# Optimization experiments

Hardware: AMD Instinct MI355X
Metric: run time of the kernel (lower is better)

Reference implementation:

```python
import jax, jax.numpy as jnp
import numpy as np

EPSILON = 0.1
ITERATIONS = 5
GAMMA = 0.1
TAU = 0.005
NEG = -1000000.0
DELTA = 1e-9


def setup_inputs() -> dict:
    key = jax.random.key(0)
    kv, kt, klv, klt = jax.random.split(key, 4)
    B, n_v, n_t, dim = 64, 512, 512, 768
    v = jax.random.normal(kv, (B, n_v, dim), dtype=jnp.float32)
    t = jax.random.normal(kt, (B, n_t, dim), dtype=jnp.float32)
    # realistic length-based masks (prefix-valid tokens), at least half valid
    len_v = jax.random.randint(klv, (B,), n_v // 2, n_v + 1)
    len_t = jax.random.randint(klt, (B,), n_t // 2, n_t + 1)
    v_mask = jnp.arange(n_v)[None, :] < len_v[:, None]
    t_mask = jnp.arange(n_t)[None, :] < len_t[:, None]
    return {"v": v, "t": t, "v_mask": v_mask, "t_mask": t_mask}


def _l2norm(x):
    return x / jnp.sqrt(jnp.sum(x * x, axis=-1, keepdims=True)).clip(1e-12)


def reference(v, t, v_mask, t_mask):
    B, n_v, dim = v.shape
    n_t = t.shape[1]
    # cosine similarity scores: [B, n_v, n_t]
    A = jnp.einsum("bvd,btd->bvt", _l2norm(v), _l2norm(t)).astype(jnp.float32)
    A_raw = A
    A = jnp.where(v_mask[:, :, None], A, NEG)
    A = jnp.where(t_mask[:, None, :], A, NEG)

    gamma = jnp.float32(GAMMA)
    def augment(M):
        M = jnp.concatenate([M, jnp.full((B, n_v, 1), gamma, M.dtype)], axis=2)
        M = jnp.concatenate([M, jnp.full((B, 1, n_t + 1), gamma, M.dtype)], axis=1)
        return M
    A_aug = augment(A)          # [B, n_v+1, n_t+1]
    A_aug_raw = augment(A_raw)

    mu_real = v_mask.astype(jnp.float32) / (v_mask.sum(axis=1, keepdims=True) + 1e-9)
    nu_real = t_mask.astype(jnp.float32) / (t_mask.sum(axis=1, keepdims=True) + 1e-9)
    ones = jnp.ones((B, 1), jnp.float32)
    mu = jnp.concatenate([mu_real, ones], axis=1)  # [B, n_v+1]
    nu = jnp.concatenate([nu_real, ones], axis=1)  # [B, n_t+1]

    K = A_aug / EPSILON
    log_mu = jnp.log(mu + 1e-9)
    log_nu = jnp.log(nu + 1e-9)

    def step(carry, _):
        u, vv = carry
        u = log_mu - jax.nn.logsumexp(K + vv[:, None, :], axis=2)
        vv = log_nu - jax.nn.logsumexp(K + u[:, :, None], axis=1)
        return (u, vv), None

    u0 = jnp.zeros_like(mu)
    v0 = jnp.zeros_like(nu)
    (u, vv), _ = jax.lax.scan(step, (u0, v0), None, length=ITERATIONS)

    log_T = u[:, :, None] + vv[:, None, :] + K
    T_star = jnp.exp(log_T)
    loss = jnp.sum(T_star * (1.0 - A_aug_raw), axis=(1, 2))

    T_real = T_star[:, :n_v, :n_t]
    T_hat = jax.nn.relu(T_real - TAU)
    w_v_num = T_hat.sum(axis=2) + DELTA
    w_v = w_v_num / w_v_num.sum(axis=1, keepdims=True)
    w_t_num = T_hat.sum(axis=1) + DELTA
    w_t = w_t_num / w_t_num.sum(axis=1, keepdims=True)
    return (loss.mean(), w_v, w_t)
```

## Files before the change

### kernel.cpp

```cpp
#include <hip/hip_runtime.h>
#include <hip/hip_fp16.h>

#define TAU_OT   0.005f
#define DELTA_OT 1e-9f
#define LOG2E    1.4426950408889634f
#define C_EPS    0.06931471805599453f
#define LM9_2    -29.897352853986263f
#define NEGI     -1.0e30f
#define SCALE_B  14.426950408889634f

constexpr int BB  = 64;
constexpr int DIM = 768;
constexpr int KP_H = 520;
constexpr long KB_H = (long)512 * KP_H;

constexpr size_t OFF_LENV = 0;
constexpr size_t OFF_LENT = 64;
constexpr size_t OFF_SCAL = 128;
constexpr size_t OFF_LOSSA= 384;
constexpr size_t OFF_SRU  = 448;
constexpr size_t OFF_SRV  = 512;
constexpr size_t OFF_U    = 576;
constexpr size_t OFF_VV   = OFF_U   + 32768;
constexpr size_t OFF_WVA  = OFF_VV  + 32768;
constexpr size_t OFF_WTA  = OFF_WVA + 32768;
constexpr size_t OFF_KH   = OFF_WTA + 32768;

typedef __attribute__((ext_vector_type(8))) short short8;
typedef __attribute__((ext_vector_type(4))) float floatx4;

__device__ inline float ex2(float x){ float r; asm("v_exp_f32 %0, %1" : "=v"(r) : "v"(x)); return r; }
__device__ inline float lg2(float x){ float r; asm("v_log_f32 %0, %1" : "=v"(r) : "v"(x)); return r; }
__device__ inline unsigned cvtpk(float a, float b){
    unsigned r; asm("v_cvt_pk_bf16_f32 %0, %1, %2" : "=v"(r) : "v"(a), "v"(b)); return r;
}

__device__ inline int detect_mode(const unsigned char* p) {
    unsigned char b0 = p[0], b1 = p[1];
    if (b0 == 0) return 2;
    return (b1 != 0) ? 0 : 1;
}
__device__ inline int read_mask(const unsigned char* p, long idx, int mode) {
    if (mode == 0) return p[idx] != 0;
    if (mode == 1) return p[4*idx] != 0;
    return ((const float*)p)[idx] != 0.0f;
}

__device__ inline void map_bs(int bid, int& b, int& s) {
    b = (bid & 7) * 8 + ((bid >> 3) & 7);
    s = bid >> 6;
}

__global__ void len_init(const unsigned char* vm, const unsigned char* tm,
                         int* LENV, int* LENT, float* VV, float* SCAL,
                         float* WTA, float* LOSSA, float* SRU) {
    int b = blockIdx.x;
    bool isV = (blockIdx.y == 0);
    const unsigned char* p = isV ? vm : tm;
    int mode = detect_mode(p);
    int i = threadIdx.x;
    float s = (float)read_mask(p, (long)b*512 + i, mode);
    #pragma unroll
    for (int off = 32; off; off >>= 1) s += __shfl_xor(s, off);
    __shared__ float wsum[8];
    int w = i >> 6, lane = i & 63;
    if (lane == 0) wsum[w] = s;
    __syncthreads();
    float len = 0.f;
    #pragma unroll
    for (int q = 0; q < 8; ++q) len += wsum[q];
    int ln = (int)(len + 0.5f);
    if (isV) {
        if (i == 0) {
            LENV[b] = ln;
            SCAL[b*4+2] = 0.f; SCAL[b*4+3] = 0.f;
            LOSSA[b] = 0.f; SRU[b] = 0.f;
        }
    } else {
        if (i == 0) LENT[b] = ln;
        VV[b*512 + i] = (i < ln) ? 0.f : NEGI;
        WTA[b*512 + i] = 0.f;
    }
}

__global__ __launch_bounds__(256) void gemm_kernel(const float* __restrict__ v,
        const float* __restrict__ t,
        const int* __restrict__ lenvp, const int* __restrict__ lentp,
        __half* __restrict__ K) {
    int bid = blockIdx.x;
    int xcd = bid & 7, kk = bid >> 3;
    int bt   = xcd * 8 + (kk >> 4);
    int tile = kk & 15;
    int m0 = (tile >> 2) * 128, n0 = (tile & 3) * 128;
    if (m0 >= lenvp[bt] || n0 >= lentp[bt]) return;

    __shared__ ushort As[128*40];
    __shared__ ushort Bs[128*40];
    __shared__ float invA[128], invB[128];
    const float* vb = v + (long)bt * 512 * DIM;
    const float* tb = t + (long)bt * 512 * DIM;
    int tid = threadIdx.x;
    int w = tid >> 6, lane = tid & 63;
    int wm = (w >> 1) * 64, wn = (w & 1) * 64;
    int lrow = lane & 15, khalf = lane >> 4;

    floatx4 acc[4][4] = {};
    float ssA[4] = {0,0,0,0}, ssB[4] = {0,0,0,0};

    for (int kt = 0; kt < DIM/32; ++kt) {
        int k0 = kt * 32;
        float4 av[4], bv[4];
        #pragma unroll
        for (int h = 0; h < 4; ++h) {
            int f = tid + h*256;
            int row = f >> 3, c4 = (f & 7) * 4;
            av[h] = *(const float4*)(vb + (long)(m0+row)*DIM + k0 + c4);
            bv[h] = *(const float4*)(tb + (long)(n0+row)*DIM + k0 + c4);
            ssA[h] += av[h].x*av[h].x + av[h].y*av[h].y + av[h].z*av[h].z + av[h].w*av[h].w;
            ssB[h] += bv[h].x*bv[h].x + bv[h].y*bv[h].y + bv[h].z*bv[h].z + bv[h].w*bv[h].w;
        }
        __syncthreads();
        #pragma unroll
        for (int h = 0; h < 4; ++h) {
            int f = tid + h*256;
            int row = f >> 3, c4 = (f & 7) * 4;
            uint2 ua = { cvtpk(av[h].x, av[h].y), cvtpk(av[h].z, av[h].w) };
            uint2 ub = { cvtpk(bv[h].x, bv[h].y), cvtpk(bv[h].z, bv[h].w) };
            *(uint2*)&As[row*40 + c4] = ua;
            *(uint2*)&Bs[row*40 + c4] = ub;
        }
        __syncthreads();
        short8 af[4], bf[4];
        #pragma unroll
        for (int mi = 0; mi < 4; ++mi)
            af[mi] = *(const short8*)&As[(wm + mi*16 + lrow)*40 + khalf*8];
        #pragma unroll
        for (int nj = 0; nj < 4; ++nj)
            bf[nj] = *(const short8*)&Bs[(wn + nj*16 + lrow)*40 + khalf*8];
        #pragma unroll
        for (int mi = 0; mi < 4; ++mi)
            #pragma unroll
            for (int nj = 0; nj < 4; ++nj)
                acc[mi][nj] = __builtin_amdgcn_mfma_f32_16x16x32_bf16(
                                  af[mi], bf[nj], acc[mi][nj], 0, 0, 0);
        __syncthreads();
    }

    #pragma unroll
    for (int h = 0; h < 4; ++h) {
        float sa = ssA[h], sb = ssB[h];
        #pragma unroll
        for (int off = 1; off < 8; off <<= 1) {
            sa += __shfl_xor(sa, off);
            sb += __shfl_xor(sb, off);
        }
        if ((tid & 7) == 0) {
            int r = (tid >> 3) + 32*h;
            invA[r] = 1.0f / fmaxf(sqrtf(sa), 1e-12f);
            invB[r] = SCALE_B / fmaxf(sqrtf(sb), 1e-12f);
        }
    }
    __syncthreads();

    __half* Kb = K + (long)bt * KB_H;
    int col = lane & 15, rq = lane >> 4;
    #pragma unroll
    for (int nj = 0; nj < 4; ++nj) {
        int gnl = wn + nj*16 + col;
        float sn = invB[gnl];
        #pragma unroll
        for (int mi = 0; mi < 4; ++mi) {
            #pragma unroll
            for (int r = 0; r < 4; ++r) {
                int gml = wm + mi*16 + rq*4 + r;
                float val = acc[mi][nj][r] * invA[gml] * sn;
                Kb[(long)(m0+gml)*KP_H + (n0+gnl)] = __float2half(val);
            }
        }
    }
}

__global__ __launch_bounds__(256) void row_kernel(const __half* __restrict__ K,
        const float* __restrict__ VV, float* __restrict__ U, float* __restrict__ SCAL,
        const int* __restrict__ LENV, const int* __restrict__ LENT) {
    int b, s; map_bs(blockIdx.x, b, s);
    int lenv = LENV[b], lent = LENT[b];
    __shared__ float vvs[512];
    int tid = threadIdx.x;
    *(float2*)&vvs[tid*2] = *(const float2*)&VV[b*512 + tid*2];
    float vv_aug = SCAL[b*4+2], vv_m = SCAL[b*4+3];
    __syncthreads();
    int w = tid >> 6, lane = tid & 63;
    int base = s*64 + w*16;
    float lmu2 = lg2(1.0f/((float)lenv + 1e-9f) + 1e-9f);
    float ea = ex2(LOG2E + vv_aug);
    const __half* Kb = K + (long)b * KB_H;
    int nr = min(16, max(0, lenv - base));
    #pragma unroll 2
    for (int r = 0; r < nr; ++r) {
        int i = base + r;
        const __half2* Kr = (const __half2*)(Kb + (long)i * KP_H);
        float ss = 0.f;
        #pragma unroll
        for (int c = 0; c < 4; ++c) {
            __half2 h2 = Kr[c*64 + lane];
            int j0 = c*128 + lane*2;
            ss += ex2(__low2float(h2) + vvs[j0]) + ex2(__high2float(h2) + vvs[j0+1]);
        }
        #pragma unroll
        for (int off = 32; off; off >>= 1) ss += __shfl_xor(ss, off);
        if (lane == 0) U[b*512 + i] = lmu2 - lg2(ss + ea);
    }
    if (lane == 0)
        for (int r = nr; r < 16; ++r) U[b*512 + base + r] = NEGI;
    if (s == 0 && w == 3) {
        float sv = 0.f;
        #pragma unroll
        for (int c = 0; c < 8; ++c) sv += ex2(vvs[c*64 + lane]);
        #pragma unroll
        for (int off = 32; off; off >>= 1) sv += __shfl_xor(sv, off);
        if (lane == 0) {
            float tot = sv + (float)(512 - lent)*ex2(vv_m) + ex2(vv_aug);
            SCAL[b*4+0] = -(LOG2E + lg2(tot));
            SCAL[b*4+1] = LM9_2 - LOG2E - vv_aug;
        }
    }
}

__global__ __launch_bounds__(256) void col_kernel(const __half* __restrict__ K,
        const float* __restrict__ U, float* __restrict__ VV, float* __restrict__ SCAL,
        const int* __restrict__ LENV, const int* __restrict__ LENT) {
    int b, s; map_bs(blockIdx.x, b, s);
    int lenv = LENV[b], lent = LENT[b];
    __shared__ float us[512];
    __shared__ float part[4][64];
    int tid = threadIdx.x;
    *(float2*)&us[tid*2] = *(const float2*)&U[b*512 + tid*2];
    float u_aug = SCAL[b*4+0], u_m = SCAL[b*4+1];
    __syncthreads();
    int w = tid >> 6, lane = tid & 63;
    int j = s*64 + lane;
    int chunk = ((lenv + 31) >> 5) << 3;
    int i0 = w*chunk, i1 = min(lenv, i0 + chunk);
    const __half* p = K + (long)b*KB_H + (long)i0*KP_H + j;
    float acc = 0.f;
    int i = i0;
    for (; i + 8 <= i1; i += 8) {
        float x[8];
        #pragma unroll
        for (int q = 0; q < 8; ++q) x[q] = __half2float(p[(long)q*KP_H]) + us[i+q];
        #pragma unroll
        for (int q = 0; q < 8; ++q) acc += ex2(x[q]);
        p += 8*KP_H;
    }
    for (; i < i1; ++i) { acc += ex2(__half2float(*p) + us[i]); p += KP_H; }
    part[w][lane] = acc;
    __syncthreads();
    if (w == 0) {
        float tot = part[0][lane] + part[1][lane] + part[2][lane] + part[3][lane]
                  + ex2(LOG2E + u_aug);
        float lnu2 = lg2(1.0f/((float)lent + 1e-9f) + 1e-9f);
        VV[b*512 + j] = (j < lent) ? (lnu2 - lg2(tot)) : NEGI;
    } else if (w == 1 && s == 0) {
        float su = 0.f;
        #pragma unroll
        for (int c = 0; c < 8; ++c) su += ex2(us[c*64 + lane]);
        #pragma unroll
        for (int off = 32; off; off >>= 1) su += __shfl_xor(su, off);
        if (lane == 0) {
            float tot = su + (float)(512 - lenv)*ex2(u_m) + ex2(u_aug);
            SCAL[b*4+2] = -(LOG2E + lg2(tot));
            SCAL[b*4+3] = LM9_2 - LOG2E - u_aug;
        }
    }
}

__global__ __launch_bounds__(256) void final_partial(const __half* __restrict__ K,
        const float* __restrict__ U, const float* __restrict__ VV,
        float* __restrict__ WVA, float* __restrict__ WTA,
        float* __restrict__ LOSSA, float* __restrict__ SRU, float* __restrict__ SRV,
        const int* __restrict__ LENV) {
    int b, s; map_bs(blockIdx.x, b, s);
    int lenv = LENV[b];
    __shared__ float vvs[512];
    __shared__ float colsum[512];
    __shared__ float lw[4];
    int tid = threadIdx.x;
    *(float2*)&vvs[tid*2] = *(const float2*)&VV[b*512 + tid*2];
    colsum[tid] = 0.f; colsum[tid+256] = 0.f;
    __syncthreads();
    int w = tid >> 6, lane = tid & 63;
    int base = s*64 + w*16;
    const __half* Kb = K + (long)b * KB_H;
    float creg[8] = {0,0,0,0,0,0,0,0};
    float lossacc = 0.f;
    int nr = min(16, max(0, lenv - base));
    for (int r = 0; r < nr; ++r) {
        int i = base + r;
        float ui = U[b*512 + i];
        const __half2* Kr = (const __half2*)(Kb + (long)i * KP_H);
        float rowacc = 0.f;
        #pragma unroll
        for (int c = 0; c < 4; ++c) {
            __half2 h2 = Kr[c*64 + lane];
            int j0 = c*128 + lane*2;
            float k0 = __low2float(h2), k1 = __high2float(h2);
            float t0 = ex2(ui + vvs[j0]   + k0);
            float t1 = ex2(ui + vvs[j0+1] + k1);
            lossacc += t0*(1.f - C_EPS*k0) + t1*(1.f - C_EPS*k1);
            float th0 = fmaxf(t0 - TAU_OT, 0.f), th1 = fmaxf(t1 - TAU_OT, 0.f);
            rowacc += th0 + th1;
            creg[2*c] += th0; creg[2*c+1] += th1;
        }
        #pragma unroll
        for (int off = 32; off; off >>= 1) rowacc += __shfl_xor(rowacc, off);
        if (lane == 0) WVA[b*512 + i] = rowacc;
    }
    if (lane == 0)
        for (int r = nr; r < 16; ++r) WVA[b*512 + base + r] = 0.f;
    #pragma unroll
    for (int c = 0; c < 4; ++c) {
        atomicAdd(&colsum[c*128 + lane*2    ], creg[2*c]);
        atomicAdd(&colsum[c*128 + lane*2 + 1], creg[2*c+1]);
    }
    #pragma unroll
    for (int off = 32; off; off >>= 1) lossacc += __shfl_xor(lossacc, off);
    if (lane == 0) lw[w] = lossacc;
    if (w == 1) {
        float e = ex2(U[b*512 + s*64 + lane]);
        #pragma unroll
        for (int off = 32; off; off >>= 1) e += __shfl_xor(e, off);
        if (lane == 0) atomicAdd(&SRU[b], e);
    }
    if (w == 2 && s == 0) {
        float sv = 0.f;
        #pragma unroll
        for (int c = 0; c < 8; ++c) sv += ex2(vvs[c*64 + lane]);
        #pragma unroll
        for (int off = 32; off; off >>= 1) sv += __shfl_xor(sv, off);
        if (lane == 0) SRV[b] = sv;
    }
    __syncthreads();
    atomicAdd(&WTA[b*512 + tid],       colsum[tid]);
    atomicAdd(&WTA[b*512 + tid + 256], colsum[tid + 256]);
    if (tid == 0) atomicAdd(&LOSSA[b], lw[0]+lw[1]+lw[2]+lw[3]);
}

__global__ void wnorm_kernel(const float* __restrict__ num, float* __restrict__ out) {
    int b = blockIdx.x;
    float v = num[b*512 + threadIdx.x] + DELTA_OT;
    float s = v;
    #pragma unroll
    for (int off = 32; off; off >>= 1) s += __shfl_xor(s, off);
    __shared__ float wsum[8];
    int w = threadIdx.x >> 6, lane = threadIdx.x & 63;
    if (lane == 0) wsum[w] = s;
    __syncthreads();
    float tot = 0.f;
    #pragma unroll
    for (int q = 0; q < 8; ++q) tot += wsum[q];
    out[b*512 + threadIdx.x] = v / tot;
}

__global__ void loss_final(const float* __restrict__ LOSSA, const float* __restrict__ SRU,
        const float* __restrict__ SRV, const float* __restrict__ SCAL,
        const int* __restrict__ LENV, const int* __restrict__ LENT,
        float* __restrict__ out) {
    int b = threadIdx.x;
    float u_aug = SCAL[b*4+0], u_m = SCAL[b*4+1];
    float vv_aug = SCAL[b*4+2], vv_m = SCAL[b*4+3];
    float lenv = (float)LENV[b], lent = (float)LENT[b];
    float laug = 0.9f * ( ex2(vv_aug + LOG2E) * (SRU[b] + (512.f - lenv)*ex2(u_m))
                        + ex2(u_aug  + LOG2E) * (SRV[b] + (512.f - lent)*ex2(vv_m))
                        + ex2(u_aug + vv_aug + LOG2E) );
    float tot = LOSSA[b] + laug;
    #pragma unroll
    for (int off = 32; off; off >>= 1) tot += __shfl_xor(tot, off);
    if (b == 0) out[0] = tot * (1.0f/64.0f);
}

extern "C" void kernel_launch(void* const* d_in, const int* in_sizes, int n_in,
                              void* d_out, int out_size, void* d_ws, size_t ws_size,
                              hipStream_t stream) {
    const float* v = (const float*)d_in[0];
    const float* t = (const float*)d_in[1];
    const unsigned char* vm = (const unsigned char*)d_in[2];
    const unsigned char* tm = (const unsigned char*)d_in[3];
    float* ws  = (float*)d_ws;
    float* out = (float*)d_out;

    int*   LENV = (int*)(ws + OFF_LENV);
    int*   LENT = (int*)(ws + OFF_LENT);
    float* SCAL = ws + OFF_SCAL;
    float* LOSSA= ws + OFF_LOSSA;
    float* SRU  = ws + OFF_SRU;
    float* SRV  = ws + OFF_SRV;
    float* U    = ws + OFF_U;
    float* VV   = ws + OFF_VV;
    float* WVA  = ws + OFF_WVA;
    float* WTA  = ws + OFF_WTA;
    __half* Kmat = (__half*)(ws + OFF_KH);

    len_init<<<dim3(BB, 2), 512, 0, stream>>>(vm, tm, LENV, LENT, VV, SCAL, WTA, LOSSA, SRU);
    gemm_kernel<<<dim3(1024), 256, 0, stream>>>(v, t, LENV, LENT, Kmat);

    for (int it = 0; it < 5; ++it) {
        row_kernel<<<dim3(512), 256, 0, stream>>>(Kmat, VV, U, SCAL, LENV, LENT);
        col_kernel<<<dim3(512), 256, 0, stream>>>(Kmat, U, VV, SCAL, LENV, LENT);
    }

    final_partial<<<dim3(512), 256, 0, stream>>>(Kmat, U, VV, WVA, WTA, LOSSA, SRU, SRV, LENV);
    wnorm_kernel<<<BB, 512, 0, stream>>>(WVA, out + 1);
    wnorm_kernel<<<BB, 512, 0, stream>>>(WTA, out + 1 + (long)BB*512);
    loss_final<<<1, 64, 0, stream>>>(LOSSA, SRU, SRV, SCAL, LENV, LENT, out);
}
```

Baseline: 378.8 us.

## Fuse Sinkhorn iterations and finalization into one cooperative kernel; double-buffer GEMM

Replaces the ten row/col kernel launches, the final partial kernel, the two normalization kernels and the loss kernel with a single cooperative kernel that uses grid.sync between phases. This removes launch overhead and inter-kernel gaps. The GEMM now double-buffers shared memory with register prefetch of the next k-slice, drops one barrier per iteration, and adds an occupancy hint. It also removes the early exit for fully masked tiles, so padded tiles are now computed too. Grid-wide syncs have their own cost and need all 512 blocks to be co-resident.

Measured after the change: 1.004 ms. 165% more time.

```diff
diff --git a/kernel.cpp b/kernel.cpp
--- a/kernel.cpp
+++ b/kernel.cpp
@@ -1,5 +1,8 @@
 #include <hip/hip_runtime.h>
 #include <hip/hip_fp16.h>
+#include <hip/hip_cooperative_groups.h>
+
+namespace cg = cooperative_groups;
 
 #define TAU_OT   0.005f
 #define DELTA_OT 1e-9f
@@ -83,67 +86,72 @@
     }
 }
 
-__global__ __launch_bounds__(256) void gemm_kernel(const float* __restrict__ v,
-        const float* __restrict__ t,
-        const int* __restrict__ lenvp, const int* __restrict__ lentp,
-        __half* __restrict__ K) {
+__global__ __launch_bounds__(256, 3) void gemm_kernel(const float* __restrict__ v,
+        const float* __restrict__ t, __half* __restrict__ K) {
     int bid = blockIdx.x;
     int xcd = bid & 7, kk = bid >> 3;
     int bt   = xcd * 8 + (kk >> 4);
     int tile = kk & 15;
     int m0 = (tile >> 2) * 128, n0 = (tile & 3) * 128;
-    if (m0 >= lenvp[bt] || n0 >= lentp[bt]) return;
-
-    __shared__ ushort As[128*40];
-    __shared__ ushort Bs[128*40];
+
+    __shared__ ushort As[2][128*40];
+    __shared__ ushort Bs[2][128*40];
     __shared__ float invA[128], invB[128];
+
     const float* vb = v + (long)bt * 512 * DIM;
     const float* tb = t + (long)bt * 512 * DIM;
     int tid = threadIdx.x;
     int w = tid >> 6, lane = tid & 63;
     int wm = (w >> 1) * 64, wn = (w & 1) * 64;
     int lrow = lane & 15, khalf = lane >> 4;
-
+    int r0 = tid >> 3, c4 = (tid & 7) * 4;
+
+    const float* pa = vb + (long)(m0 + r0) * DIM + c4;
+    const float* pb = tb + (long)(n0 + r0) * DIM + c4;
+
+    float4 av[4], bv[4];
+    #pragma unroll
+    for (int h = 0; h < 4; ++h) {
+        av[h] = *(const float4*)(pa + (long)(32*h) * DIM);
+        bv[h] = *(const float4*)(pb + (long)(32*h) * DIM);
+    }
+    float ssA[4] = {0,0,0,0}, ssB[4] = {0,0,0,0};
     floatx4 acc[4][4] = {};
-    float ssA[4] = {0,0,0,0}, ssB[4] = {0,0,0,0};
-
-    for (int kt = 0; kt < DIM/32; ++kt) {
-        int k0 = kt * 32;
-        float4 av[4], bv[4];
+
+    for (int kt = 0; kt < 24; ++kt) {
+        ushort* Ac = &As[kt & 1][0];
+        ushort* Bc = &Bs[kt & 1][0];
         #pragma unroll
         for (int h = 0; h < 4; ++h) {
-            int f = tid + h*256;
-            int row = f >> 3, c4 = (f & 7) * 4;
-            av[h] = *(const float4*)(vb + (long)(m0+row)*DIM + k0 + c4);
-            bv[h] = *(const float4*)(tb + (long)(n0+row)*DIM + k0 + c4);
             ssA[h] += av[h].x*av[h].x + av[h].y*av[h].y + av[h].z*av[h].z + av[h].w*av[h].w;
             ssB[h] += bv[h].x*bv[h].x + bv[h].y*bv[h].y + bv[h].z*bv[h].z + bv[h].w*bv[h].w;
-        }
-        __syncthreads();
-        #pragma unroll
-        for (int h = 0; h < 4; ++h) {
-            int f = tid + h*256;
-            int row = f >> 3, c4 = (f & 7) * 4;
             uint2 ua = { cvtpk(av[h].x, av[h].y), cvtpk(av[h].z, av[h].w) };
             uint2 ub = { cvtpk(bv[h].x, bv[h].y), cvtpk(bv[h].z, bv[h].w) };
-            *(uint2*)&As[row*40 + c4] = ua;
-            *(uint2*)&Bs[row*40 + c4] = ub;
+            *(uint2*)&Ac[(r0 + 32*h)*40 + c4] = ua;
+            *(uint2*)&Bc[(r0 + 32*h)*40 + c4] = ub;
+        }
+        if (kt < 23) {
+            int k0 = (kt + 1) * 32;
+            #pragma unroll
+            for (int h = 0; h < 4; ++h) {
+                av[h] = *(const float4*)(pa + (long)(32*h) * DIM + k0);
+                bv[h] = *(const float4*)(pb + (long)(32*h) * DIM + k0);
+            }
         }
         __syncthreads();
         short8 af[4], bf[4];
         #pragma unroll
         for (int mi = 0; mi < 4; ++mi)
-            af[mi] = *(const short8*)&As[(wm + mi*16 + lrow)*40 + khalf*8];
+            af[mi] = *(const short8*)&Ac[(wm + mi*16 + lrow)*40 + khalf*8];
         #pragma unroll
         for (int nj = 0; nj < 4; ++nj)
-            bf[nj] = *(const short8*)&Bs[(wn + nj*16 + lrow)*40 + khalf*8];
+            bf[nj] = *(const short8*)&Bc[(wn + nj*16 + lrow)*40 + khalf*8];
         #pragma unroll
         for (int mi = 0; mi < 4; ++mi)
             #pragma unroll
             for (int nj = 0; nj < 4; ++nj)
                 acc[mi][nj] = __builtin_amdgcn_mfma_f32_16x16x32_bf16(
                                   af[mi], bf[nj], acc[mi][nj], 0, 0, 0);
-        __syncthreads();
     }
 
     #pragma unroll
@@ -155,9 +163,8 @@
             sb += __shfl_xor(sb, off);
         }
         if ((tid & 7) == 0) {
-            int r = (tid >> 3) + 32*h;
-            invA[r] = 1.0f / fmaxf(sqrtf(sa), 1e-12f);
-            invB[r] = SCALE_B / fmaxf(sqrtf(sb), 1e-12f);
+            invA[r0 + 32*h] = 1.0f / fmaxf(sqrtf(sa), 1e-12f);
+            invB[r0 + 32*h] = SCALE_B / fmaxf(sqrtf(sb), 1e-12f);
         }
     }
     __syncthreads();
@@ -180,203 +187,191 @@
     }
 }
 
-__global__ __launch_bounds__(256) void row_kernel(const __half* __restrict__ K,
-        const float* __restrict__ VV, float* __restrict__ U, float* __restrict__ SCAL,
-        const int* __restrict__ LENV, const int* __restrict__ LENT) {
+__global__ __launch_bounds__(256, 2) void sink_coop(const __half* __restrict__ K,
+        float* __restrict__ U, float* __restrict__ VV, float* __restrict__ SCAL,
+        const int* __restrict__ LENV, const int* __restrict__ LENT,
+        float* __restrict__ WVA, float* __restrict__ WTA, float* __restrict__ LOSSA,
+        float* __restrict__ SRU, float* __restrict__ SRV, float* __restrict__ out) {
+    cg::grid_group grid = cg::this_grid();
     int b, s; map_bs(blockIdx.x, b, s);
     int lenv = LENV[b], lent = LENT[b];
-    __shared__ float vvs[512];
-    int tid = threadIdx.x;
-    *(float2*)&vvs[tid*2] = *(const float2*)&VV[b*512 + tid*2];
-    float vv_aug = SCAL[b*4+2], vv_m = SCAL[b*4+3];
-    __syncthreads();
-    int w = tid >> 6, lane = tid & 63;
-    int base = s*64 + w*16;
+    int tid = threadIdx.x, w = tid >> 6, lane = tid & 63;
+    const __half* Kb = K + (long)b * KB_H;
+
+    __shared__ float sv[512];
+    __shared__ float aux[512];
+    __shared__ float part[4][64];
+    __shared__ float lw[16];
+
     float lmu2 = lg2(1.0f/((float)lenv + 1e-9f) + 1e-9f);
-    float ea = ex2(LOG2E + vv_aug);
-    const __half* Kb = K + (long)b * KB_H;
-    int nr = min(16, max(0, lenv - base));
-    #pragma unroll 2
-    for (int r = 0; r < nr; ++r) {
-        int i = base + r;
-        const __half2* Kr = (const __half2*)(Kb + (long)i * KP_H);
-        float ss = 0.f;
+    float lnu2 = lg2(1.0f/((float)lent + 1e-9f) + 1e-9f);
+
+    for (int it = 0; it < 5; ++it) {
+        {
+            *(float2*)&sv[tid*2] = *(const float2*)&VV[b*512 + tid*2];
+            float vv_aug = SCAL[b*4+2], vv_m = SCAL[b*4+3];
+            __syncthreads();
+            int base = s*64 + w*16;
+            float ea = ex2(LOG2E + vv_aug);
+            int nr = min(16, max(0, lenv - base));
+            for (int r = 0; r < nr; ++r) {
+                int i = base + r;
+                const __half2* Kr = (const __half2*)(Kb + (long)i * KP_H);
+                float ss = 0.f;
+                #pragma unroll
+                for (int c = 0; c < 4; ++c) {
+                    __half2 h2 = Kr[c*64 + lane];
+                    int j0 = c*128 + lane*2;
+                    ss += ex2(__low2float(h2) + sv[j0]) + ex2(__high2float(h2) + sv[j0+1]);
+                }
+                #pragma unroll
+                for (int off = 32; off; off >>= 1) ss += __shfl_xor(ss, off);
+                if (lane == 0) U[b*512 + i] = lmu2 - lg2(ss + ea);
+            }
+            if (lane == 0)
+                for (int r = nr; r < 16; ++r) U[b*512 + base + r] = NEGI;
+            if (s == 0 && w == 3) {
+                float svv = 0.f;
+                #pragma unroll
+                for (int c = 0; c < 8; ++c) svv += ex2(sv[c*64 + lane]);
+                #pragma unroll
+                for (int off = 32; off; off >>= 1) svv += __shfl_xor(svv, off);
+                if (lane == 0) {
+                    float tot = svv + (float)(512 - lent)*ex2(vv_m) + ex2(vv_aug);
+                    SCAL[b*4+0] = -(LOG2E + lg2(tot));
+                    SCAL[b*4+1] = LM9_2 - LOG2E - vv_aug;
+                }
+            }
+        }
+        grid.sync();
+        {
+            *(float2*)&sv[tid*2] = *(const float2*)&U[b*512 + tid*2];
+            float u_aug = SCAL[b*4+0], u_m = SCAL[b*4+1];
+            __syncthreads();
+            int j = s*64 + lane;
+            int chunk = ((lenv + 31) >> 5) << 3;
+            int i0 = w*chunk, i1 = min(lenv, i0 + chunk);
+            const __half* p = Kb + (long)i0*KP_H + j;
+            float acc = 0.f;
+            int i = i0;
+            for (; i + 8 <= i1; i += 8) {
+                float x[8];
+                #pragma unroll
+                for (int q = 0; q < 8; ++q) x[q] = __half2float(p[(long)q*KP_H]) + sv[i+q];
+                #pragma unroll
+                for (int q = 0; q < 8; ++q) acc += ex2(x[q]);
+                p += 8*KP_H;
+            }
+            for (; i < i1; ++i) { acc += ex2(__half2float(*p) + sv[i]); p += KP_H; }
+            part[w][lane] = acc;
+            __syncthreads();
+            if (w == 0) {
+                float tot = part[0][lane] + part[1][lane] + part[2][lane] + part[3][lane]
+                          + ex2(LOG2E + u_aug);
+                VV[b*512 + j] = (j < lent) ? (lnu2 - lg2(tot)) : NEGI;
+            } else if (w == 1 && s == 0) {
+                float su = 0.f;
+                #pragma unroll
+                for (int c = 0; c < 8; ++c) su += ex2(sv[c*64 + lane]);
+                #pragma unroll
+                for (int off = 32; off; off >>= 1) su += __shfl_xor(su, off);
+                if (lane == 0) {
+                    float tot = su + (float)(512 - lenv)*ex2(u_m) + ex2(u_aug);
+                    SCAL[b*4+2] = -(LOG2E + lg2(tot));
+                    SCAL[b*4+3] = LM9_2 - LOG2E - u_aug;
+                }
+            }
+        }
+        grid.sync();
+    }
+
+    {
+        *(float2*)&sv[tid*2] = *(const float2*)&VV[b*512 + tid*2];
+        aux[tid] = 0.f; aux[tid + 256] = 0.f;
+        __syncthreads();
+        int base = s*64 + w*16;
+        float creg[8] = {0,0,0,0,0,0,0,0};
+        float lossacc = 0.f;
+        int nr = min(16, max(0, lenv - base));
+        for (int r = 0; r < nr; ++r) {
+            int i = base + r;
+            float ui = U[b*512 + i];
+            const __half2* Kr = (const __half2*)(Kb + (long)i * KP_H);
+            float rowacc = 0.f;
+            #pragma unroll
+            for (int c = 0; c < 4; ++c) {
+                __half2 h2 = Kr[c*64 + lane];
+                int j0 = c*128 + lane*2;
+                float k0 = __low2float(h2), k1 = __high2float(h2);
+                float t0 = ex2(ui + sv[j0]   + k0);
+                float t1 = ex2(ui + sv[j0+1] + k1);
+                lossacc += t0*(1.f - C_EPS*k0) + t1*(1.f - C_EPS*k1);
+                float th0 = fmaxf(t0 - TAU_OT, 0.f), th1 = fmaxf(t1 - TAU_OT, 0.f);
+                rowacc += th0 + th1;
+                creg[2*c] += th0; creg[2*c+1] += th1;
+            }
+            #pragma unroll
+            for (int off = 32; off; off >>= 1) rowacc += __shfl_xor(rowacc, off);
+            if (lane == 0) WVA[b*512 + i] = rowacc;
+        }
+        if (lane == 0)
+            for (int r = nr; r < 16; ++r) WVA[b*512 + base + r] = 0.f;
         #pragma unroll
         for (int c = 0; c < 4; ++c) {
-            __half2 h2 = Kr[c*64 + lane];
-            int j0 = c*128 + lane*2;
-            ss += ex2(__low2float(h2) + vvs[j0]) + ex2(__high2float(h2) + vvs[j0+1]);
-        }
-        #pragma unroll
-        for (int off = 32; off; off >>= 1) ss += __shfl_xor(ss, off);
-        if (lane == 0) U[b*512 + i] = lmu2 - lg2(ss + ea);
-    }
-    if (lane == 0)
-        for (int r = nr; r < 16; ++r) U[b*512 + base + r] = NEGI;
-    if (s == 0 && w == 3) {
-        float sv = 0.f;
-        #pragma unroll
-        for (int c = 0; c < 8; ++c) sv += ex2(vvs[c*64 + lane]);
-        #pragma unroll
-        for (int off = 32; off; off >>= 1) sv += __shfl_xor(sv, off);
-        if (lane == 0) {
-            float tot = sv + (float)(512 - lent)*ex2(vv_m) + ex2(vv_aug);
-            SCAL[b*4+0] = -(LOG2E + lg2(tot));
-            SCAL[b*4+1] = LM9_2 - LOG2E - vv_aug;
-        }
-    }
-}
-
-__global__ __launch_bounds__(256) void col_kernel(const __half* __restrict__ K,
-        const float* __restrict__ U, float* __restrict__ VV, float* __restrict__ SCAL,
-        const int* __restrict__ LENV, const int* __restrict__ LENT) {
-    int b, s; map_bs(blockIdx.x, b, s);
-    int lenv = LENV[b], lent = LENT[b];
-    __shared__ float us[512];
-    __shared__ float part[4][64];
-    int tid = threadIdx.x;
-    *(float2*)&us[tid*2] = *(const float2*)&U[b*512 + tid*2];
-    float u_aug = SCAL[b*4+0], u_m = SCAL[b*4+1];
-    __syncthreads();
-    int w = tid >> 6, lane = tid & 63;
-    int j = s*64 + lane;
-    int chunk = ((lenv + 31) >> 5) << 3;
-    int i0 = w*chunk, i1 = min(lenv, i0 + chunk);
-    const __half* p = K + (long)b*KB_H + (long)i0*KP_H + j;
-    float acc = 0.f;
-    int i = i0;
-    for (; i + 8 <= i1; i += 8) {
-        float x[8];
-        #pragma unroll
-        for (int q = 0; q < 8; ++q) x[q] = __half2float(p[(long)q*KP_H]) + us[i+q];
-        #pragma unroll
-        for (int q = 0; q < 8; ++q) acc += ex2(x[q]);
-        p += 8*KP_H;
-    }
-    for (; i < i1; ++i) { acc += ex2(__half2float(*p) + us[i]); p += KP_H; }
-    part[w][lane] = acc;
-    __syncthreads();
-    if (w == 0) {
-        float tot = part[0][lane] + part[1][lane] + part[2][lane] + part[3][lane]
-                  + ex2(LOG2E + u_aug);
-        float lnu2 = lg2(1.0f/((float)lent + 1e-9f) + 1e-9f);
-        VV[b*512 + j] = (j < lent) ? (lnu2 - lg2(tot)) : NEGI;
-    } else if (w == 1 && s == 0) {
-        float su = 0.f;
-        #pragma unroll
-        for (int c = 0; c < 8; ++c) su += ex2(us[c*64 + lane]);
-        #pragma unroll
-        for (int off = 32; off; off >>= 1) su += __shfl_xor(su, off);
-        if (lane == 0) {
-            float tot = su + (float)(512 - lenv)*ex2(u_m) + ex2(u_aug);
-            SCAL[b*4+2] = -(LOG2E + lg2(tot));
-            SCAL[b*4+3] = LM9_2 - LOG2E - u_aug;
-        }
-    }
-}
-
-__global__ __launch_bounds__(256) void final_partial(const __half* __restrict__ K,
-        const float* __restrict__ U, const float* __restrict__ VV,
-        float* __restrict__ WVA, float* __restrict__ WTA,
-        float* __restrict__ LOSSA, float* __restrict__ SRU, float* __restrict__ SRV,
-        const int* __restrict__ LENV) {
-    int b, s; map_bs(blockIdx.x, b, s);
-    int lenv = LENV[b];
-    __shared__ float vvs[512];
-    __shared__ float colsum[512];
-    __shared__ float lw[4];
-    int tid = threadIdx.x;
-    *(float2*)&vvs[tid*2] = *(const float2*)&VV[b*512 + tid*2];
-    colsum[tid] = 0.f; colsum[tid+256] = 0.f;
-    __syncthreads();
-    int w = tid >> 6, lane = tid & 63;
-    int base = s*64 + w*16;
-    const __half* Kb = K + (long)b * KB_H;
-    float creg[8] = {0,0,0,0,0,0,0,0};
-    float lossacc = 0.f;
-    int nr = min(16, max(0, lenv - base));
-    for (int r = 0; r < nr; ++r) {
-        int i = base + r;
-        float ui = U[b*512 + i];
-        const __half2* Kr = (const __half2*)(Kb + (long)i * KP_H);
-        float rowacc = 0.f;
-        #pragma unroll
-        for (int c = 0; c < 4; ++c) {
-            __half2 h2 = Kr[c*64 + lane];
-            int j0 = c*128 + lane*2;
-            float k0 = __low2float(h2), k1 = __high2float(h2);
-            float t0 = ex2(ui + vvs[j0]   + k0);
-            float t1 = ex2(ui + vvs[j0+1] + k1);
-            lossacc += t0*(1.f - C_EPS*k0) + t1*(1.f - C_EPS*k1);
-            float th0 = fmaxf(t0 - TAU_OT, 0.f), th1 = fmaxf(t1 - TAU_OT, 0.f);
-            rowacc += th0 + th1;
-            creg[2*c] += th0; creg[2*c+1] += th1;
-        }
-        #pragma unroll
-        for (int off = 32; off; off >>= 1) rowacc += __shfl_xor(rowacc, off);
-        if (lane == 0) WVA[b*512 + i] = rowacc;
-    }
-    if (lane == 0)
-        for (int r = nr; r < 16; ++r) WVA[b*512 + base + r] = 0.f;
-    #pragma unroll
-    for (int c = 0; c < 4; ++c) {
-        atomicAdd(&colsum[c*128 + lane*2    ], creg[2*c]);
-        atomicAdd(&colsum[c*128 + lane*2 + 1], creg[2*c+1]);
-    }
-    #pragma unroll
-    for (int off = 32; off; off >>= 1) lossacc += __shfl_xor(lossacc, off);
-    if (lane == 0) lw[w] = lossacc;
-    if (w == 1) {
-        float e = ex2(U[b*512 + s*64 + lane]);
-        #pragma unroll
-        for (int off = 32; off; off >>= 1) e += __shfl_xor(e, off);
-        if (lane == 0) atomicAdd(&SRU[b], e);
-    }
-    if (w == 2 && s == 0) {
-        float sv = 0.f;
-        #pragma unroll
-        for (int c = 0; c < 8; ++c) sv += ex2(vvs[c*64 + lane]);
-        #pragma unroll
-        for (int off = 32; off; off >>= 1) sv += __shfl_xor(sv, off);
-        if (lane == 0) SRV[b] = sv;
-    }
-    __syncthreads();
-    atomicAdd(&WTA[b*512 + tid],       colsum[tid]);
-    atomicAdd(&WTA[b*512 + tid + 256], colsum[tid + 256]);
-    if (tid == 0) atomicAdd(&LOSSA[b], lw[0]+lw[1]+lw[2]+lw[3]);
-}
-
-__global__ void wnorm_kernel(const float* __restrict__ num, float* __restrict__ out) {
-    int b = blockIdx.x;
-    float v = num[b*512 + threadIdx.x] + DELTA_OT;
-    float s = v;
-    #pragma unroll
-    for (int off = 32; off; off >>= 1) s += __shfl_xor(s, off);
-    __shared__ float wsum[8];
-    int w = threadIdx.x >> 6, lane = threadIdx.x & 63;
-    if (lane == 0) wsum[w] = s;
-    __syncthreads();
-    float tot = 0.f;
-    #pragma unroll
-    for (int q = 0; q < 8; ++q) tot += wsum[q];
-    out[b*512 + threadIdx.x] = v / tot;
-}
-
-__global__ void loss_final(const float* __restrict__ LOSSA, const float* __restrict__ SRU,
-        const float* __restrict__ SRV, const float* __restrict__ SCAL,
-        const int* __restrict__ LENV, const int* __restrict__ LENT,
-        float* __restrict__ out) {
-    int b = threadIdx.x;
-    float u_aug = SCAL[b*4+0], u_m = SCAL[b*4+1];
-    float vv_aug = SCAL[b*4+2], vv_m = SCAL[b*4+3];
-    float lenv = (float)LENV[b], lent = (float)LENT[b];
-    float laug = 0.9f * ( ex2(vv_aug + LOG2E) * (SRU[b] + (512.f - lenv)*ex2(u_m))
-                        + ex2(u_aug  + LOG2E) * (SRV[b] + (512.f - lent)*ex2(vv_m))
-                        + ex2(u_aug + vv_aug + LOG2E) );
-    float tot = LOSSA[b] + laug;
-    #pragma unroll
-    for (int off = 32; off; off >>= 1) tot += __shfl_xor(tot, off);
-    if (b == 0) out[0] = tot * (1.0f/64.0f);
+            atomicAdd(&aux[c*128 + lane*2    ], creg[2*c]);
+            atomicAdd(&aux[c*128 + lane*2 + 1], creg[2*c+1]);
+        }
+        #pragma unroll
+        for (int off = 32; off; off >>= 1) lossacc += __shfl_xor(lossacc, off);
+        if (lane == 0) lw[w] = lossacc;
+        if (w == 1) {
+            float e = ex2(U[b*512 + s*64 + lane]);
+            #pragma unroll
+            for (int off = 32; off; off >>= 1) e += __shfl_xor(e, off);
+            if (lane == 0) atomicAdd(&SRU[b], e);
+        }
+        if (w == 2 && s == 0) {
+            float svv = 0.f;
+            #pragma unroll
+            for (int c = 0; c < 8; ++c) svv += ex2(sv[c*64 + lane]);
+            #pragma unroll
+            for (int off = 32; off; off >>= 1) svv += __shfl_xor(svv, off);
+            if (lane == 0) SRV[b] = svv;
+        }
+        __syncthreads();
+        atomicAdd(&WTA[b*512 + tid],       aux[tid]);
+        atomicAdd(&WTA[b*512 + tid + 256], aux[tid + 256]);
+        if (tid == 0) atomicAdd(&LOSSA[b], lw[0]+lw[1]+lw[2]+lw[3]);
+    }
+    grid.sync();
+
+    if (blockIdx.x < 128) {
+        int bb = blockIdx.x & 63;
+        const float* num = (blockIdx.x < 64) ? WVA : WTA;
+        float* dst = out + 1 + ((blockIdx.x < 64) ? 0L : (long)BB*512) + (long)bb*512;
+        float v0 = num[bb*512 + tid] + DELTA_OT;
+        float v1 = num[bb*512 + tid + 256] + DELTA_OT;
+        float ssum = v0 + v1;
+        #pragma unroll
+        for (int off = 32; off; off >>= 1) ssum += __shfl_xor(ssum, off);
+        if (lane == 0) lw[w] = ssum;
+        __syncthreads();
+        float tot = lw[0] + lw[1] + lw[2] + lw[3];
+        dst[tid] = v0 / tot;
+        dst[tid + 256] = v1 / tot;
+    } else if (blockIdx.x == 128 && tid < 64) {
+        int bq = tid;
+        float u_aug = SCAL[bq*4+0], u_m = SCAL[bq*4+1];
+        float vv_aug = SCAL[bq*4+2], vv_m = SCAL[bq*4+3];
+        float flv = (float)LENV[bq], flt = (float)LENT[bq];
+        float laug = 0.9f * ( ex2(vv_aug + LOG2E) * (SRU[bq] + (512.f - flv)*ex2(u_m))
+                            + ex2(u_aug  + LOG2E) * (SRV[bq] + (512.f - flt)*ex2(vv_m))
+                            + ex2(u_aug + vv_aug + LOG2E) );
+        float tot = LOSSA[bq] + laug;
+        #pragma unroll
+        for (int off = 32; off; off >>= 1) tot += __shfl_xor(tot, off);
+        if (tid == 0) out[0] = tot * (1.0f/64.0f);
+    }
 }
 
 extern "C" void kernel_launch(void* const* d_in, const int* in_sizes, int n_in,
@@ -402,15 +397,14 @@
     __half* Kmat = (__half*)(ws + OFF_KH);
 
     len_init<<<dim3(BB, 2), 512, 0, stream>>>(vm, tm, LENV, LENT, VV, SCAL, WTA, LOSSA, SRU);
-    gemm_kernel<<<dim3(1024), 256, 0, stream>>>(v, t, LENV, LENT, Kmat);
-
-    for (int it = 0; it < 5; ++it) {
-        row_kernel<<<dim3(512), 256, 0, stream>>>(Kmat, VV, U, SCAL, LENV, LENT);
-        col_kernel<<<dim3(512), 256, 0, stream>>>(Kmat, U, VV, SCAL, LENV, LENT);
-    }
-
-    final_partial<<<dim3(512), 256, 0, stream>>>(Kmat, U, VV, WVA, WTA, LOSSA, SRU, SRV, LENV);
-    wnorm_kernel<<<BB, 512, 0, stream>>>(WVA, out + 1);
-    wnorm_kernel<<<BB, 512, 0, stream>>>(WTA, out + 1 + (long)BB*512);
-    loss_final<<<1, 64, 0, stream>>>(LOSSA, SRU, SRV, SCAL, LENV, LENT, out);
-}
+    gemm_kernel<<<dim3(1024), 256, 0, stream>>>(v, t, Kmat);
+
+    const __half* Kc = Kmat;
+    const int* LENVc = LENV;
+    const int* LENTc = LENT;
+    void* args[] = { (void*)&Kc, (void*)&U, (void*)&VV, (void*)&SCAL,
+                     (void*)&LENVc, (void*)&LENTc, (void*)&WVA, (void*)&WTA,
+                     (void*)&LOSSA, (void*)&SRU, (void*)&SRV, (void*)&out };
+    hipLaunchCooperativeKernel((const void*)sink_coop, dim3(512), dim3(256),
+                               args, 0, stream);
+}
```
